# Optimization experiments

Measured on AMD Instinct MI355X. Metric: run time of the kernel, lower is better.

Reference implementation:

```python
import jax, jax.numpy as jnp
import numpy as np
from jax.ops import segment_sum, segment_max

N_NODES = 100000
N_EDGES = 1600000


def _glorot(key, shape):
    fan_in, fan_out = shape[0], shape[-1]
    lim = np.sqrt(6.0 / (fan_in + fan_out))
    return jax.random.uniform(key, shape, jnp.float32, -lim, lim)


def setup_inputs() -> dict:
    key = jax.random.key(0)
    ks = jax.random.split(key, 12)
    x = jax.random.normal(ks[0], (N_NODES, 7), jnp.float32)
    edge_index = jax.random.randint(ks[1], (2, N_EDGES), 0, N_NODES, jnp.int64)
    return {
        "x": x,
        "edge_index": edge_index,
        # GCNConv(7, 32)
        "W1": _glorot(ks[2], (7, 32)), "b1": jnp.zeros((32,), jnp.float32),
        # GATConv(32, 64), heads=1
        "W2": _glorot(ks[3], (32, 64)), "a_src2": _glorot(ks[4], (64, 1))[:, 0],
        "a_dst2": _glorot(ks[5], (64, 1))[:, 0], "b2": jnp.zeros((64,), jnp.float32),
        # GCNConv(64, 128)
        "W3": _glorot(ks[6], (64, 128)), "b3": jnp.zeros((128,), jnp.float32),
        # GATConv(128, 2), heads=1
        "W4": _glorot(ks[7], (128, 2)), "a_src4": _glorot(ks[8], (2, 1))[:, 0],
        "a_dst4": _glorot(ks[9], (2, 1))[:, 0], "b4": jnp.zeros((2,), jnp.float32),
    }


def _gcn_conv(x, src, dst, W, b):
    # x' = W x; symmetric normalization with self-loops already in (src, dst)
    h = x @ W
    deg = segment_sum(jnp.ones_like(dst, dtype=h.dtype), dst, num_segments=N_NODES)
    dinv = jnp.where(deg > 0, jax.lax.rsqrt(deg), 0.0)
    norm = dinv[src] * dinv[dst]            # [E]
    msg = norm[:, None] * h[src]            # [E, C]
    return segment_sum(msg, dst, num_segments=N_NODES) + b


def _gat_conv(x, src, dst, W, a_src, a_dst, b, slope=0.2):
    h = x @ W                               # [N, C]
    alpha_src = h @ a_src                   # [N]
    alpha_dst = h @ a_dst                   # [N]
    e = alpha_src[src] + alpha_dst[dst]     # [E]
    e = jnp.where(e > 0, e, slope * e)      # leaky_relu
    # numerically-stable softmax over edges grouped by destination node
    m = segment_max(e, dst, num_segments=N_NODES)
    ex = jnp.exp(e - m[dst])
    denom = segment_sum(ex, dst, num_segments=N_NODES)
    w = ex / (denom[dst] + 1e-16)           # [E]
    out = segment_sum(w[:, None] * h[src], dst, num_segments=N_NODES)
    return out + b


def reference(x, edge_index, W1, b1, W2, a_src2, a_dst2, b2, W3, b3, W4, a_src4, a_dst4, b4):
    # add self-loops once (PyG does it per layer; identical edge set each time)
    loop = jnp.arange(N_NODES, dtype=edge_index.dtype)
    src = jnp.concatenate([edge_index[0], loop])
    dst = jnp.concatenate([edge_index[1], loop])

    h = _gcn_conv(x, src, dst, W1, b1)
    h = jax.nn.relu(h)
    h = _gat_conv(h, src, dst, W2, a_src2, a_dst2, b2)
    h = jax.nn.relu(h)
    h = _gcn_conv(h, src, dst, W3, b3)
    h = jax.nn.relu(h)
    h = _gat_conv(h, src, dst, W4, a_src4, a_dst4, b4)
    return jax.nn.log_softmax(h, axis=1)
```

## Files before the change

kernel.cpp:

```cpp
#include <hip/hip_runtime.h>
#include <hip/hip_bf16.h>

#define NN 100000
#define NE 1600000
#define NT (NN + NE)
#define NBKT 256
#define BSZ 391
#define BCAP 10240

typedef unsigned int u32;
typedef unsigned short u16;

static __device__ __forceinline__ int clampN(int s) {
    return ((unsigned)s < (unsigned)NN) ? s : 0;
}
static __device__ __forceinline__ int ld_src(const int* ei, int is32, int e) {
    return is32 ? ei[e] : ei[2 * e];
}
static __device__ __forceinline__ int ld_dst(const int* ei, int is32, int e) {
    return is32 ? ei[NE + e] : ei[2 * NE + 2 * e];
}
static __device__ __forceinline__ float2 b2x2(u32 u) {
    float2 r;
    r.x = __uint_as_float((u & 0xffffu) << 16);
    r.y = __uint_as_float(u & 0xffff0000u);
    return r;
}
static __device__ __forceinline__ u16 f2bs(float f) {
    union { __hip_bfloat16 b; u16 u; } cv;
    cv.b = __float2bfloat16(f);
    return cv.u;
}
static __device__ __forceinline__ u32 pack2(float x, float y) {
    return ((u32)f2bs(y) << 16) | (u32)f2bs(x);
}
static __device__ __forceinline__ float lrelu_c(float e) {
    e = (e > 0.f) ? e : 0.2f * e;
    return fminf(e, 60.f);
}

#define FMA4(acc, s, v) { acc.x += (s)*(v).x; acc.y += (s)*(v).y; \
                          acc.z += (s)*(v).z; acc.w += (s)*(v).w; }


__global__ void __launch_bounds__(256) k_init(const float* __restrict__ W2,
                                              const float* __restrict__ a2s,
                                              const float* __restrict__ a2d,
                                              const int* __restrict__ ei,
                                              float* __restrict__ va2,
                                              float* __restrict__ vd2,
                                              int* __restrict__ flag,
                                              int* __restrict__ gcur) {
    if (blockIdx.x == 0) {
        if (threadIdx.x == 0) flag[0] = 0;
        __syncthreads();
        int nz = 0;
        for (int i = threadIdx.x; i < 4096; i += 256) nz |= ei[2 * i + 1];
        if (nz) atomicOr(flag, 1);
        if (threadIdx.x < NBKT) gcur[threadIdx.x] = 0;
    } else if (threadIdx.x < 64) {
        int t = threadIdx.x;
        if (t < 32) {
            float a = 0.f;
            for (int c = 0; c < 64; c++) a += W2[t * 64 + c] * a2s[c];
            va2[t] = a;
        } else {
            int k = t - 32;
            float a = 0.f;
            for (int c = 0; c < 64; c++) a += W2[k * 64 + c] * a2d[c];
            vd2[k] = a;
        }
    }
}


__global__ void __launch_bounds__(256) k_binA(const int* __restrict__ ei,
                                              const int* __restrict__ flag,
                                              int* __restrict__ gcur,
                                              u32* __restrict__ staging) {
    __shared__ int hist[NBKT];
    __shared__ int gbase[NBKT];
    __shared__ int cnt2[NBKT];
    int tid = threadIdx.x;
    if (tid < NBKT) hist[tid] = 0;
    __syncthreads();

    int base = blockIdx.x * 4096;
    int is32 = flag[0];
    int d[16], s[16];
    #pragma unroll
    for (int i = 0; i < 16; i++) {
        int e = base + i * 256 + tid;
        d[i] = -1;
        if (e < NE) {
            int dd = ld_dst(ei, is32, e);
            if ((unsigned)dd < (unsigned)NN) { d[i] = dd; s[i] = clampN(ld_src(ei, is32, e)); }
        } else if (e < NT) {
            d[i] = e - NE; s[i] = e - NE;
        }
        if (d[i] >= 0) atomicAdd(&hist[d[i] / BSZ], 1);
    }
    __syncthreads();
    if (tid < NBKT) {
        int c = hist[tid];
        gbase[tid] = c ? atomicAdd(&gcur[tid], c) : 0;
        cnt2[tid] = 0;
    }
    __syncthreads();
    #pragma unroll
    for (int i = 0; i < 16; i++) {
        if (d[i] >= 0) {
            int b = d[i] / BSZ;
            int pos = gbase[b] + atomicAdd(&cnt2[b], 1);
            if (pos < BCAP)
                staging[(size_t)b * BCAP + pos] =
                    ((unsigned)(d[i] - b * BSZ) << 17) | (unsigned)s[i];
        }
    }
}

__global__ void __launch_bounds__(256) k_histscan(const u32* __restrict__ staging,
                                                  const int* __restrict__ gcur,
                                                  const float* __restrict__ x,
                                                  u32* __restrict__ xpb,
                                                  int* __restrict__ rowptr,
                                                  int* __restrict__ deg,
                                                  int* __restrict__ part) {
    __shared__ int h[512];
    __shared__ int sm[256];
    int b = blockIdx.x, tid = threadIdx.x;
    h[tid] = 0; h[tid + 256] = 0;
    __syncthreads();
    int cnt = min(gcur[b], BCAP);
    const u32* st = staging + (size_t)b * BCAP;
    for (int i = tid; i < cnt; i += 256)
        atomicAdd(&h[st[i] >> 17], 1);
    __syncthreads();
    int h0 = h[2 * tid], h1 = h[2 * tid + 1];
    int pair = h0 + h1;
    sm[tid] = pair;
    __syncthreads();
    for (int off = 1; off < 256; off <<= 1) {
        int t = (tid >= off) ? sm[tid - off] : 0;
        __syncthreads();
        sm[tid] += t;
        __syncthreads();
    }
    int excl = sm[tid] - pair;
    int g0 = b * BSZ + 2 * tid;
    if (2 * tid < BSZ && g0 < NN) { rowptr[g0] = excl; deg[g0] = h0; }
    int g1 = g0 + 1;
    if (2 * tid + 1 < BSZ && g1 < NN) { rowptr[g1] = excl + h0; deg[g1] = h1; }
    if (tid == 255) part[b] = sm[255];

    for (int i = b * 256 + tid; i < NN * 4; i += NBKT * 256) {
        int n = i >> 2, c2 = i & 3;
        float f0 = x[n * 7 + 2 * c2];
        float f1 = (2 * c2 + 1 < 7) ? x[n * 7 + 2 * c2 + 1] : 0.f;
        xpb[i] = pack2(f0, f1);
    }
}

__global__ void __launch_bounds__(256) k_scat(const u32* __restrict__ staging,
                                              const int* __restrict__ gcur,
                                              const int* __restrict__ part,
                                              int* __restrict__ rowptr,
                                              const int* __restrict__ deg,
                                              float* __restrict__ dinv,
                                              int* __restrict__ col) {
    __shared__ int sm[256];
    __shared__ int cur[BSZ];
    int b = blockIdx.x, tid = threadIdx.x;
    int v = part[tid];
    sm[tid] = v;
    __syncthreads();
    for (int off = 1; off < 256; off <<= 1) {
        int t = (tid >= off) ? sm[tid - off] : 0;
        __syncthreads();
        sm[tid] += t;
        __syncthreads();
    }
    int pb = (b > 0) ? sm[b - 1] : 0;
    if (b == 0 && tid == 0) rowptr[NN] = NT;
    for (int l = tid; l < BSZ; l += 256) {
        int g = b * BSZ + l;
        if (g < NN) {
            int r = rowptr[g] + pb;
            rowptr[g] = r;
            cur[l] = r;
            int d = deg[g];
            dinv[g] = rsqrtf((float)(d > 0 ? d : 1));
        } else cur[l] = 0;
    }
    __syncthreads();
    int cnt = min(gcur[b], BCAP);
    const u32* st = staging + (size_t)b * BCAP;
    for (int i = tid; i < cnt; i += 256) {
        u32 w = st[i];
        int l = w >> 17;
        int s = w & 0x1FFFF;
        int p = atomicAdd(&cur[l], 1);
        if ((unsigned)p < (unsigned)NT) col[p] = s;
    }
}


__global__ void __launch_bounds__(256) k_l1(const u32* __restrict__ xpb,
                                            const int* __restrict__ rowptr,
                                            const int* __restrict__ col,
                                            const float* __restrict__ dinv,
                                            const float* __restrict__ W1,
                                            const float* __restrict__ b1,
                                            const float* __restrict__ va2,
                                            const float* __restrict__ vd2,
                                            u32* __restrict__ O1b,
                                            float* __restrict__ as_,
                                            float* __restrict__ ad_) {
    __shared__ float sW1[7 * 32];
    __shared__ float sb1[32], sva[32], svd[32];
    __shared__ float sT1[64 * 8];
    if (threadIdx.x < 224) sW1[threadIdx.x] = W1[threadIdx.x];
    else {
        int c = threadIdx.x - 224;
        sb1[c] = b1[c]; sva[c] = va2[c]; svd[c] = vd2[c];
    }
    __syncthreads();

    int node_l = threadIdx.x >> 2;
    int lane = threadIdx.x & 3;
    int n = blockIdx.x * 64 + node_l;
    if (n >= NN) return;
    {
        int beg = rowptr[n], end = rowptr[n + 1];
        float ax = 0.f, ay = 0.f;
        #pragma unroll 4
        for (int e = beg; e < end; e++) {
            int s = clampN(col[e]);
            float w = dinv[s];
            float2 f = b2x2(xpb[(size_t)s * 4 + lane]);
            ax += w * f.x;
            ay += w * f.y;
        }
        float dn = dinv[n];
        sT1[node_l * 8 + lane * 2] = ax * dn;
        sT1[node_l * 8 + lane * 2 + 1] = ay * dn;
    }
    __builtin_amdgcn_wave_barrier();
    int c8 = lane * 8;
    float4 aA = {0,0,0,0}, aB = {0,0,0,0};
    #pragma unroll
    for (int k = 0; k < 7; k++) {
        float t = sT1[node_l * 8 + k];
        float4 wva = *(const float4*)&sW1[k * 32 + c8];
        float4 wvb = *(const float4*)&sW1[k * 32 + c8 + 4];
        FMA4(aA, t, wva);
        FMA4(aB, t, wvb);
    }
    float o0 = fmaxf(aA.x + sb1[c8], 0.f);
    float o1 = fmaxf(aA.y + sb1[c8 + 1], 0.f);
    float o2 = fmaxf(aA.z + sb1[c8 + 2], 0.f);
    float o3 = fmaxf(aA.w + sb1[c8 + 3], 0.f);
    float o4 = fmaxf(aB.x + sb1[c8 + 4], 0.f);
    float o5 = fmaxf(aB.y + sb1[c8 + 5], 0.f);
    float o6 = fmaxf(aB.z + sb1[c8 + 6], 0.f);
    float o7 = fmaxf(aB.w + sb1[c8 + 7], 0.f);
    uint4 pk = {pack2(o0, o1), pack2(o2, o3), pack2(o4, o5), pack2(o6, o7)};
    *(uint4*)(O1b + (size_t)n * 16 + lane * 4) = pk;
    float vs = o0 * sva[c8] + o1 * sva[c8 + 1] + o2 * sva[c8 + 2] + o3 * sva[c8 + 3]
             + o4 * sva[c8 + 4] + o5 * sva[c8 + 5] + o6 * sva[c8 + 6] + o7 * sva[c8 + 7];
    float vd = o0 * svd[c8] + o1 * svd[c8 + 1] + o2 * svd[c8 + 2] + o3 * svd[c8 + 3]
             + o4 * svd[c8 + 4] + o5 * svd[c8 + 5] + o6 * svd[c8 + 6] + o7 * svd[c8 + 7];
    vs += __shfl_xor(vs, 1, 4); vs += __shfl_xor(vs, 2, 4);
    vd += __shfl_xor(vd, 1, 4); vd += __shfl_xor(vd, 2, 4);
    if (lane == 0) { as_[n] = vs; ad_[n] = vd; }
}


__global__ void __launch_bounds__(256) k_l2(const u32* __restrict__ O1b,
                                            const float* __restrict__ as_,
                                            const float* __restrict__ ad_,
                                            const int* __restrict__ rowptr,
                                            const int* __restrict__ col,
                                            const float* __restrict__ W2,
                                            const float* __restrict__ b2,
                                            const float* __restrict__ dinv,
                                            u32* __restrict__ O2b) {
    __shared__ float sW2[32 * 64];
    __shared__ float sT2[32 * 36];
    __shared__ float sb2[64];
    {
        const float4* g = (const float4*)W2;
        float4* s4 = (float4*)sW2;
        s4[threadIdx.x] = g[threadIdx.x];
        s4[threadIdx.x + 256] = g[threadIdx.x + 256];
    }
    if (threadIdx.x < 64) sb2[threadIdx.x] = b2[threadIdx.x];
    __syncthreads();

    int node_l = threadIdx.x >> 3;
    int lane = threadIdx.x & 7;
    int n = blockIdx.x * 32 + node_l;
    {
        int beg = rowptr[n], end = rowptr[n + 1];
        float adn = ad_[n];
        float den = 0.f;
        float4 acc = {0, 0, 0, 0};
        #pragma unroll 2
        for (int e = beg; e < end; e++) {
            int s = clampN(col[e]);
            float p = __expf(lrelu_c(as_[s] + adn));
            den += p;
            uint2 w = *(const uint2*)(O1b + (size_t)s * 16 + lane * 2);
            float2 f0 = b2x2(w.x), f1 = b2x2(w.y);
            acc.x += p * f0.x; acc.y += p * f0.y; acc.z += p * f1.x; acc.w += p * f1.y;
        }
        float inv = 1.0f / (den + 1e-16f);
        acc.x *= inv; acc.y *= inv; acc.z *= inv; acc.w *= inv;
        *(float4*)&sT2[node_l * 36 + lane * 4] = acc;
    }
    __builtin_amdgcn_wave_barrier();

    int grp = threadIdx.x >> 4;
    int l = threadIdx.x & 15;
    int c4 = l * 4;
    int lbase = grp * 2;

    float4 acc0 = {0,0,0,0}, acc1 = {0,0,0,0};
    #pragma unroll
    for (int k4 = 0; k4 < 8; k4++) {
        float4 t0 = *(const float4*)&sT2[(lbase + 0) * 36 + 4 * k4];
        float4 t1 = *(const float4*)&sT2[(lbase + 1) * 36 + 4 * k4];
        #pragma unroll
        for (int j = 0; j < 4; j++) {
            float4 wv = *(const float4*)&sW2[(4 * k4 + j) * 64 + c4];
            FMA4(acc0, ((const float*)&t0)[j], wv);
            FMA4(acc1, ((const float*)&t1)[j], wv);
        }
    }
    float4 bb = *(const float4*)&sb2[c4];
    int n0 = blockIdx.x * 32 + lbase;
    float d0 = dinv[n0], d1 = dinv[n0 + 1];
    {
        float o0 = fmaxf(acc0.x + bb.x, 0.f) * d0;
        float o1 = fmaxf(acc0.y + bb.y, 0.f) * d0;
        float o2 = fmaxf(acc0.z + bb.z, 0.f) * d0;
        float o3 = fmaxf(acc0.w + bb.w, 0.f) * d0;
        uint2 pk = {pack2(o0, o1), pack2(o2, o3)};
        *(uint2*)(O2b + (size_t)n0 * 32 + l * 2) = pk;
    }
    {
        float o0 = fmaxf(acc1.x + bb.x, 0.f) * d1;
        float o1 = fmaxf(acc1.y + bb.y, 0.f) * d1;
        float o2 = fmaxf(acc1.z + bb.z, 0.f) * d1;
        float o3 = fmaxf(acc1.w + bb.w, 0.f) * d1;
        uint2 pk = {pack2(o0, o1), pack2(o2, o3)};
        *(uint2*)(O2b + (size_t)(n0 + 1) * 32 + l * 2) = pk;
    }
}


__global__ void __launch_bounds__(512) k_l3(const u32* __restrict__ O2b,
                                            const int* __restrict__ rowptr,
                                            const int* __restrict__ col,
                                            const float* __restrict__ dinv,
                                            const float* __restrict__ W3,
                                            const float* __restrict__ b3,
                                            const float* __restrict__ W4,
                                            const float* __restrict__ av4s,
                                            const float* __restrict__ av4d,
                                            float4* __restrict__ h4as,
                                            float* __restrict__ ad_) {
    __shared__ float sW3[64 * 128];
    __shared__ float sT3[64 * 68];
    __shared__ float sW4[128 * 2];
    __shared__ float sb3[128];

    {
        const float4* g = (const float4*)W3;
        float4* s4 = (float4*)sW3;
        #pragma unroll
        for (int i = 0; i < 4; i++) s4[threadIdx.x + 512 * i] = g[threadIdx.x + 512 * i];
    }
    if (threadIdx.x < 128) {
        sb3[threadIdx.x] = b3[threadIdx.x];
        sW4[2 * threadIdx.x] = W4[2 * threadIdx.x];
        sW4[2 * threadIdx.x + 1] = W4[2 * threadIdx.x + 1];
    }
    __syncthreads();

    int w = threadIdx.x >> 6;
    int l = threadIdx.x & 63;
    int node_sub = l >> 3;
    int cl = l & 7;
    int row = w * 8 + node_sub;
    int n = blockIdx.x * 64 + row;
    if (n >= NN) return;

    {
        int beg = rowptr[n], end = rowptr[n + 1];
        float4 accA = {0,0,0,0}, accB = {0,0,0,0};
        #pragma unroll 4
        for (int e = beg; e < end; e++) {
            int s = clampN(col[e]);
            uint4 wd = *(const uint4*)(O2b + (size_t)s * 32 + cl * 4);
            float2 f0 = b2x2(wd.x), f1 = b2x2(wd.y), f2 = b2x2(wd.z), f3 = b2x2(wd.w);
            accA.x += f0.x; accA.y += f0.y; accA.z += f1.x; accA.w += f1.y;
            accB.x += f2.x; accB.y += f2.y; accB.z += f3.x; accB.w += f3.y;
        }
        float dn = dinv[n];
        accA.x *= dn; accA.y *= dn; accA.z *= dn; accA.w *= dn;
        accB.x *= dn; accB.y *= dn; accB.z *= dn; accB.w *= dn;
        float* dst = &sT3[row * 68 + cl * 8];
        *(float4*)dst = accA;
        *(float4*)(dst + 4) = accB;
    }
    __builtin_amdgcn_wave_barrier();

    const float* trow = &sT3[row * 68];
    float4 acc0 = {0,0,0,0}, acc1 = {0,0,0,0}, acc2 = {0,0,0,0}, acc3 = {0,0,0,0};
    #pragma unroll 4
    for (int k4 = 0; k4 < 16; k4++) {
        float4 t4 = *(const float4*)&trow[k4 * 4];
        #pragma unroll
        for (int j = 0; j < 4; j++) {
            float tj = ((const float*)&t4)[j];
            const float* wr = &sW3[(k4 * 4 + j) * 128 + 4 * cl];
            float4 w0 = *(const float4*)&wr[0];
            float4 w1 = *(const float4*)&wr[32];
            float4 w2 = *(const float4*)&wr[64];
            float4 w3v = *(const float4*)&wr[96];
            FMA4(acc0, tj, w0);
            FMA4(acc1, tj, w1);
            FMA4(acc2, tj, w2);
            FMA4(acc3, tj, w3v);
        }
    }

    float av4s0 = av4s[0], av4s1 = av4s[1];
    float av4d0 = av4d[0], av4d1 = av4d[1];
    float p0 = 0.f, p1 = 0.f;
    #pragma unroll
    for (int q = 0; q < 4; q++) {
        float4 a = (q == 0) ? acc0 : (q == 1) ? acc1 : (q == 2) ? acc2 : acc3;
        int c = 4 * cl + 32 * q;
        float4 bb = *(const float4*)&sb3[c];
        a.x = fmaxf(a.x + bb.x, 0.f);
        a.y = fmaxf(a.y + bb.y, 0.f);
        a.z = fmaxf(a.z + bb.z, 0.f);
        a.w = fmaxf(a.w + bb.w, 0.f);
        p0 += a.x * sW4[2 * c]     + a.y * sW4[2 * (c + 1)]
            + a.z * sW4[2 * (c + 2)] + a.w * sW4[2 * (c + 3)];
        p1 += a.x * sW4[2 * c + 1]     + a.y * sW4[2 * (c + 1) + 1]
            + a.z * sW4[2 * (c + 2) + 1] + a.w * sW4[2 * (c + 3) + 1];
    }
    p0 += __shfl_xor(p0, 1, 8); p0 += __shfl_xor(p0, 2, 8); p0 += __shfl_xor(p0, 4, 8);
    p1 += __shfl_xor(p1, 1, 8); p1 += __shfl_xor(p1, 2, 8); p1 += __shfl_xor(p1, 4, 8);
    if (cl == 0) {
        float asv = p0 * av4s0 + p1 * av4s1;
        float4 pk = {p0, p1, asv, 0.f};
        h4as[n] = pk;
        ad_[n] = p0 * av4d0 + p1 * av4d1;
    }
}


__global__ void k_final(const float4* __restrict__ h4as,
                        const float* __restrict__ ad_, const int* __restrict__ rowptr,
                        const int* __restrict__ col, const float* __restrict__ b,
                        float* __restrict__ out) {
    int gid = blockIdx.x * 256 + threadIdx.x;
    int n = gid >> 2;
    if (n >= NN) return;
    int lsub = gid & 3;
    int beg = rowptr[n], end = rowptr[n + 1];
    float adn = ad_[n];
    float den = 0.f, a0 = 0.f, a1 = 0.f;
    for (int e = beg + lsub; e < end; e += 4) {
        int s = clampN(col[e]);
        float4 h = h4as[s];
        float p = __expf(lrelu_c(h.z + adn));
        den += p;
        a0 += p * h.x;
        a1 += p * h.y;
    }
    den += __shfl_xor(den, 1, 4); den += __shfl_xor(den, 2, 4);
    a0  += __shfl_xor(a0, 1, 4);  a0  += __shfl_xor(a0, 2, 4);
    a1  += __shfl_xor(a1, 1, 4);  a1  += __shfl_xor(a1, 2, 4);
    if (lsub == 0) {
        float inv = 1.0f / (den + 1e-16f);
        float v0 = a0 * inv + b[0];
        float v1 = a1 * inv + b[1];
        float mx = fmaxf(v0, v1);
        float lse = mx + logf(__expf(v0 - mx) + __expf(v1 - mx));
        float2 o = {v0 - lse, v1 - lse};
        *(float2*)(out + n * 2) = o;
    }
}

__global__ void k_sentinel(float* __restrict__ out, float v) {
    int i = blockIdx.x * 256 + threadIdx.x;
    if (i < NN * 2) out[i] = v;
}


extern "C" void kernel_launch(void* const* d_in, const int* in_sizes, int n_in,
                              void* d_out, int out_size, void* d_ws, size_t ws_size,
                              hipStream_t stream) {
    const float* x    = (const float*)d_in[0];
    const int* ei     = (const int*)d_in[1];
    const float* W1   = (const float*)d_in[2];
    const float* b1   = (const float*)d_in[3];
    const float* W2   = (const float*)d_in[4];
    const float* a2s  = (const float*)d_in[5];
    const float* a2d  = (const float*)d_in[6];
    const float* b2   = (const float*)d_in[7];
    const float* W3   = (const float*)d_in[8];
    const float* b3   = (const float*)d_in[9];
    const float* W4   = (const float*)d_in[10];
    const float* a4s  = (const float*)d_in[11];
    const float* a4d  = (const float*)d_in[12];
    const float* b4   = (const float*)d_in[13];
    float* out = (float*)d_out;

    char* base = (char*)d_ws;
    size_t off = 0;
    auto alloc = [&](size_t bytes) {
        char* q = base + off;
        off += (bytes + 255) & ~(size_t)255;
        return q;
    };
    u32* xpb     = (u32*)alloc((size_t)NN * 4 * 4);
    u32* O1b     = (u32*)alloc((size_t)NN * 16 * 4);
    u32* O2b     = (u32*)alloc((size_t)NN * 32 * 4);
    u32* staging = (u32*)alloc((size_t)NBKT * BCAP * 4);
    int* col     = (int*)alloc((size_t)NT * 4);
    int* rowptr  = (int*)alloc((size_t)(NN + 1) * 4);
    int* deg     = (int*)alloc((size_t)NN * 4);
    float* dinv  = (float*)alloc((size_t)NN * 4);
    float* as_   = (float*)alloc((size_t)NN * 4);
    float* ad_   = (float*)alloc((size_t)NN * 4);
    float4* h4as = (float4*)alloc((size_t)NN * 16);
    int* part    = (int*)alloc(512 * 4);
    int* flag    = (int*)alloc(256);
    int* gcur    = (int*)alloc(NBKT * 4);
    float* va2   = (float*)alloc(32 * 4);
    float* vd2   = (float*)alloc(32 * 4);

    float code = 0.f;
    if (off > ws_size)            code = 1000.f + (float)(ws_size >> 20);
    else if (n_in != 14)          code = 2000.f + 10.f * (float)n_in;
    else if (out_size != NN * 2)  code = 3400.f;
    if (code != 0.f) {
        k_sentinel<<<(NN * 2 + 255) / 256, 256, 0, stream>>>(out, code);
        return;
    }

    const int NTILE = (NT + 4095) / 4096;

    k_init<<<2, 256, 0, stream>>>(W2, a2s, a2d, ei, va2, vd2, flag, gcur);
    k_binA<<<NTILE, 256, 0, stream>>>(ei, flag, gcur, staging);
    k_histscan<<<NBKT, 256, 0, stream>>>(staging, gcur, x, xpb, rowptr, deg, part);
    k_scat<<<NBKT, 256, 0, stream>>>(staging, gcur, part, rowptr, deg, dinv, col);

    k_l1<<<(NN + 63) / 64, 256, 0, stream>>>(xpb, rowptr, col, dinv,
                                             W1, b1, va2, vd2, O1b, as_, ad_);
    k_l2<<<NN / 32, 256, 0, stream>>>(O1b, as_, ad_, rowptr, col,
                                      W2, b2, dinv, O2b);
    k_l3<<<(NN + 63) / 64, 512, 0, stream>>>(O2b, rowptr, col, dinv,
                                             W3, b3, W4, a4s, a4d, h4as, ad_);
    k_final<<<NN * 4 / 256 + 1, 256, 0, stream>>>(h4as, ad_, rowptr, col, b4, out);
}
```

Measured before the change: 253.8 us.

## Split edge loops across two lane slots with wider loads and shuffle reduction

In the three CSR gather kernels, the lanes assigned to each node are split into two slots that walk alternate edges, and each lane loads twice as many bf16 features per edge using wider vector loads. The partial sums are combined with an xor shuffle and written to shared memory by one slot. This halves the serial edge-loop length per node and raises memory-level parallelism on the gathers. The cost is more registers and extra shuffle instructions.

```diff
diff --git a/kernel.cpp b/kernel.cpp
--- a/kernel.cpp
+++ b/kernel.cpp
@@ -228,22 +228,28 @@
 
     int node_l = threadIdx.x >> 2;
     int lane = threadIdx.x & 3;
+    int slot = lane >> 1;
+    int ck = lane & 1;
     int n = blockIdx.x * 64 + node_l;
     if (n >= NN) return;
     {
         int beg = rowptr[n], end = rowptr[n + 1];
-        float ax = 0.f, ay = 0.f;
-        #pragma unroll 4
-        for (int e = beg; e < end; e++) {
+        float a0 = 0.f, a1 = 0.f, a2 = 0.f, a3 = 0.f;
+        #pragma unroll 2
+        for (int e = beg + slot; e < end; e += 2) {
             int s = clampN(col[e]);
             float w = dinv[s];
-            float2 f = b2x2(xpb[(size_t)s * 4 + lane]);
-            ax += w * f.x;
-            ay += w * f.y;
-        }
-        float dn = dinv[n];
-        sT1[node_l * 8 + lane * 2] = ax * dn;
-        sT1[node_l * 8 + lane * 2 + 1] = ay * dn;
+            uint2 u = *(const uint2*)(xpb + (size_t)s * 4 + ck * 2);
+            float2 f0 = b2x2(u.x), f1 = b2x2(u.y);
+            a0 += w * f0.x; a1 += w * f0.y; a2 += w * f1.x; a3 += w * f1.y;
+        }
+        a0 += __shfl_xor(a0, 2, 4); a1 += __shfl_xor(a1, 2, 4);
+        a2 += __shfl_xor(a2, 2, 4); a3 += __shfl_xor(a3, 2, 4);
+        if (slot == 0) {
+            float dn = dinv[n];
+            float4 o = {a0 * dn, a1 * dn, a2 * dn, a3 * dn};
+            *(float4*)&sT1[node_l * 8 + ck * 4] = o;
+        }
     }
     __builtin_amdgcn_wave_barrier();
     int c8 = lane * 8;
@@ -298,25 +304,38 @@
     __syncthreads();
 
     int node_l = threadIdx.x >> 3;
-    int lane = threadIdx.x & 7;
+    int l8 = threadIdx.x & 7;
+    int slot = l8 >> 2;
+    int ck = l8 & 3;
     int n = blockIdx.x * 32 + node_l;
     {
         int beg = rowptr[n], end = rowptr[n + 1];
         float adn = ad_[n];
         float den = 0.f;
-        float4 acc = {0, 0, 0, 0};
+        float a0=0.f,a1=0.f,a2=0.f,a3=0.f,a4=0.f,a5=0.f,a6=0.f,a7=0.f;
         #pragma unroll 2
-        for (int e = beg; e < end; e++) {
+        for (int e = beg + slot; e < end; e += 2) {
             int s = clampN(col[e]);
             float p = __expf(lrelu_c(as_[s] + adn));
             den += p;
-            uint2 w = *(const uint2*)(O1b + (size_t)s * 16 + lane * 2);
-            float2 f0 = b2x2(w.x), f1 = b2x2(w.y);
-            acc.x += p * f0.x; acc.y += p * f0.y; acc.z += p * f1.x; acc.w += p * f1.y;
-        }
-        float inv = 1.0f / (den + 1e-16f);
-        acc.x *= inv; acc.y *= inv; acc.z *= inv; acc.w *= inv;
-        *(float4*)&sT2[node_l * 36 + lane * 4] = acc;
+            uint4 w = *(const uint4*)(O1b + (size_t)s * 16 + ck * 4);
+            float2 f0 = b2x2(w.x), f1 = b2x2(w.y), f2 = b2x2(w.z), f3 = b2x2(w.w);
+            a0 += p * f0.x; a1 += p * f0.y; a2 += p * f1.x; a3 += p * f1.y;
+            a4 += p * f2.x; a5 += p * f2.y; a6 += p * f3.x; a7 += p * f3.y;
+        }
+        den += __shfl_xor(den, 4, 8);
+        a0 += __shfl_xor(a0, 4, 8); a1 += __shfl_xor(a1, 4, 8);
+        a2 += __shfl_xor(a2, 4, 8); a3 += __shfl_xor(a3, 4, 8);
+        a4 += __shfl_xor(a4, 4, 8); a5 += __shfl_xor(a5, 4, 8);
+        a6 += __shfl_xor(a6, 4, 8); a7 += __shfl_xor(a7, 4, 8);
+        if (slot == 0) {
+            float inv = 1.0f / (den + 1e-16f);
+            float4 oA = {a0 * inv, a1 * inv, a2 * inv, a3 * inv};
+            float4 oB = {a4 * inv, a5 * inv, a6 * inv, a7 * inv};
+            float* dst = &sT2[node_l * 36 + ck * 8];
+            *(float4*)dst = oA;
+            *(float4*)(dst + 4) = oB;
+        }
     }
     __builtin_amdgcn_wave_barrier();
 
@@ -390,32 +409,55 @@
 
     int w = threadIdx.x >> 6;
     int l = threadIdx.x & 63;
-    int node_sub = l >> 3;
-    int cl = l & 7;
-    int row = w * 8 + node_sub;
+    int g8 = l >> 3;
+    int row = w * 8 + g8;
     int n = blockIdx.x * 64 + row;
     if (n >= NN) return;
 
     {
+        int slot = (l >> 2) & 1;
+        int ck = l & 3;
         int beg = rowptr[n], end = rowptr[n + 1];
-        float4 accA = {0,0,0,0}, accB = {0,0,0,0};
-        #pragma unroll 4
-        for (int e = beg; e < end; e++) {
+        float2 ac[8];
+        #pragma unroll
+        for (int i = 0; i < 8; i++) { ac[i].x = 0.f; ac[i].y = 0.f; }
+        #pragma unroll 2
+        for (int e = beg + slot; e < end; e += 2) {
             int s = clampN(col[e]);
-            uint4 wd = *(const uint4*)(O2b + (size_t)s * 32 + cl * 4);
-            float2 f0 = b2x2(wd.x), f1 = b2x2(wd.y), f2 = b2x2(wd.z), f3 = b2x2(wd.w);
-            accA.x += f0.x; accA.y += f0.y; accA.z += f1.x; accA.w += f1.y;
-            accB.x += f2.x; accB.y += f2.y; accB.z += f3.x; accB.w += f3.y;
-        }
-        float dn = dinv[n];
-        accA.x *= dn; accA.y *= dn; accA.z *= dn; accA.w *= dn;
-        accB.x *= dn; accB.y *= dn; accB.z *= dn; accB.w *= dn;
-        float* dst = &sT3[row * 68 + cl * 8];
-        *(float4*)dst = accA;
-        *(float4*)(dst + 4) = accB;
+            const uint4* rp = (const uint4*)(O2b + (size_t)s * 32 + ck * 8);
+            uint4 wa = rp[0];
+            uint4 wb = rp[1];
+            float2 f;
+            f = b2x2(wa.x); ac[0].x += f.x; ac[0].y += f.y;
+            f = b2x2(wa.y); ac[1].x += f.x; ac[1].y += f.y;
+            f = b2x2(wa.z); ac[2].x += f.x; ac[2].y += f.y;
+            f = b2x2(wa.w); ac[3].x += f.x; ac[3].y += f.y;
+            f = b2x2(wb.x); ac[4].x += f.x; ac[4].y += f.y;
+            f = b2x2(wb.y); ac[5].x += f.x; ac[5].y += f.y;
+            f = b2x2(wb.z); ac[6].x += f.x; ac[6].y += f.y;
+            f = b2x2(wb.w); ac[7].x += f.x; ac[7].y += f.y;
+        }
+        #pragma unroll
+        for (int i = 0; i < 8; i++) {
+            ac[i].x += __shfl_xor(ac[i].x, 4, 8);
+            ac[i].y += __shfl_xor(ac[i].y, 4, 8);
+        }
+        if (slot == 0) {
+            float dn = dinv[n];
+            float* dst = &sT3[row * 68 + ck * 16];
+            float4 o0 = {ac[0].x * dn, ac[0].y * dn, ac[1].x * dn, ac[1].y * dn};
+            float4 o1 = {ac[2].x * dn, ac[2].y * dn, ac[3].x * dn, ac[3].y * dn};
+            float4 o2 = {ac[4].x * dn, ac[4].y * dn, ac[5].x * dn, ac[5].y * dn};
+            float4 o3 = {ac[6].x * dn, ac[6].y * dn, ac[7].x * dn, ac[7].y * dn};
+            *(float4*)&dst[0]  = o0;
+            *(float4*)&dst[4]  = o1;
+            *(float4*)&dst[8]  = o2;
+            *(float4*)&dst[12] = o3;
+        }
     }
     __builtin_amdgcn_wave_barrier();
 
+    int cl = l & 7;
     const float* trow = &sT3[row * 68];
     float4 acc0 = {0,0,0,0}, acc1 = {0,0,0,0}, acc2 = {0,0,0,0}, acc3 = {0,0,0,0};
     #pragma unroll 4
```

Measured after the change: 252.8 us. Within noise of the previous version (-0.4%).
